# Performance work log

Hardware: AMD Instinct MI355X
Metric: run time of the kernel (lower is better)

Reference implementation:

```python
import jax, jax.numpy as jnp
import numpy as np

CHUNK_SIZE = 64  # matches init_kwargs chunk_size


def setup_inputs() -> dict:
    key = jax.random.key(0)
    g = jax.random.normal(key, (16, 16384, 64), dtype=jnp.float32)  # [B, T, H]
    return {"g": g}


def reference(g) -> jnp.ndarray:
    # Chunk-local cumsum along T: each chunk of CHUNK_SIZE has an independent
    # inclusive prefix sum (no carry across chunks), matching the torch loop.
    B, T, H = g.shape
    n_chunks = T // CHUNK_SIZE  # T chosen as multiple of CHUNK_SIZE
    gc = g.reshape(B, n_chunks, CHUNK_SIZE, H)
    out = jnp.cumsum(gc, axis=2).reshape(B, T, H).astype(jnp.float32)
    return out
```

## Files before the change

### kernel.cpp

```cpp
#include <hip/hip_runtime.h>


__global__ __launch_bounds__(256) void chunk_cumsum_kernel(
    const float4* __restrict__ g, float4* __restrict__ out) {
    const int tid = blockIdx.x * blockDim.x + threadIdx.x;
    const int h4  = tid & 15;
    const long col = tid >> 4;
    const long base = col * 1024 + h4;
    const float4* gp = g + base;
    float4*       op = out + base;

    float4 acc;
    acc.x = 0.f; acc.y = 0.f; acc.z = 0.f; acc.w = 0.f;

#pragma unroll
    for (int t = 0; t < 64; ++t) {
        float4 v = gp[(long)t * 16];
        acc.x += v.x; acc.y += v.y; acc.z += v.z; acc.w += v.w;
        op[(long)t * 16] = acc;
    }
}

extern "C" void kernel_launch(void* const* d_in, const int* in_sizes, int n_in,
                              void* d_out, int out_size, void* d_ws, size_t ws_size,
                              hipStream_t stream) {
    const float4* g  = (const float4*)d_in[0];
    float4*       out = (float4*)d_out;
    const int threads = 256;
    const int blocks  = 65536 / threads;
    chunk_cumsum_kernel<<<blocks, threads, 0, stream>>>(g, out);
}
```

Baseline: 29.79 us.

## Split each chunk across four lanes with wave-shuffle scan to raise parallelism

Each 64-step chunk column is now split into four 16-row segments handled by separate lane groups. Each lane loads its 16 float4 values up front, does a local prefix sum, and combines segment totals with two shuffle-up steps. This gives four times as many threads and more independent loads in flight per thread, aiming to hide memory latency in a bandwidth-bound kernel. The cost is more registers per thread (launch bounds now request occupancy 4) and a small amount of shuffle work.

```diff
diff --git a/kernel.cpp b/kernel.cpp
--- a/kernel.cpp
+++ b/kernel.cpp
@@ -1,32 +1,64 @@
 #include <hip/hip_runtime.h>
 
 
-__global__ __launch_bounds__(256) void chunk_cumsum_kernel(
+__global__ __launch_bounds__(256, 4) void chunk_cumsum_kernel(
     const float4* __restrict__ g, float4* __restrict__ out) {
     const int tid = blockIdx.x * blockDim.x + threadIdx.x;
     const int h4  = tid & 15;
-    const long col = tid >> 4;
-    const long base = col * 1024 + h4;
+    const int q   = (tid >> 4) & 3;
+    const long col = tid >> 6;
+
+    const long base = col * 1024 + (long)q * 256 + h4;
     const float4* gp = g + base;
     float4*       op = out + base;
 
-    float4 acc;
-    acc.x = 0.f; acc.y = 0.f; acc.z = 0.f; acc.w = 0.f;
+    float4 v[16];
+#pragma unroll
+    for (int t = 0; t < 16; ++t) v[t] = gp[(long)t * 16];
 
 #pragma unroll
-    for (int t = 0; t < 64; ++t) {
-        float4 v = gp[(long)t * 16];
-        acc.x += v.x; acc.y += v.y; acc.z += v.z; acc.w += v.w;
-        op[(long)t * 16] = acc;
+    for (int t = 1; t < 16; ++t) {
+        v[t].x += v[t - 1].x; v[t].y += v[t - 1].y;
+        v[t].z += v[t - 1].z; v[t].w += v[t - 1].w;
+    }
+
+    float4 tot = v[15];
+    float4 c;  c.x = 0.f; c.y = 0.f; c.z = 0.f; c.w = 0.f;
+
+    float4 u1;
+    u1.x = __shfl_up(tot.x, 16, 64);
+    u1.y = __shfl_up(tot.y, 16, 64);
+    u1.z = __shfl_up(tot.z, 16, 64);
+    u1.w = __shfl_up(tot.w, 16, 64);
+    float4 p = tot;
+    if (q >= 1) {
+        c.x += u1.x; c.y += u1.y; c.z += u1.z; c.w += u1.w;
+        p.x += u1.x; p.y += u1.y; p.z += u1.z; p.w += u1.w;
+    }
+    float4 u2;
+    u2.x = __shfl_up(p.x, 32, 64);
+    u2.y = __shfl_up(p.y, 32, 64);
+    u2.z = __shfl_up(p.z, 32, 64);
+    u2.w = __shfl_up(p.w, 32, 64);
+    if (q >= 2) {
+        c.x += u2.x; c.y += u2.y; c.z += u2.z; c.w += u2.w;
+    }
+
+#pragma unroll
+    for (int t = 0; t < 16; ++t) {
+        float4 r;
+        r.x = v[t].x + c.x; r.y = v[t].y + c.y;
+        r.z = v[t].z + c.z; r.w = v[t].w + c.w;
+        op[(long)t * 16] = r;
     }
 }
 
 extern "C" void kernel_launch(void* const* d_in, const int* in_sizes, int n_in,
                               void* d_out, int out_size, void* d_ws, size_t ws_size,
                               hipStream_t stream) {
-    const float4* g  = (const float4*)d_in[0];
+    const float4* g   = (const float4*)d_in[0];
     float4*       out = (float4*)d_out;
     const int threads = 256;
-    const int blocks  = 65536 / threads;
+    const int blocks  = 262144 / threads;
     chunk_cumsum_kernel<<<blocks, threads, 0, stream>>>(g, out);
 }
```

New measurement: 26.10 us. 1.14x faster.
